# Kernel optimization log

Hardware: AMD Instinct MI355X
Metric: run time of the kernel (lower is better)

Reference implementation:

```python
import jax, jax.numpy as jnp
import numpy as np
from itertools import product

H, W, BINS = 480, 640, 10
B, N_PER = 8, 250000


def setup_inputs() -> dict:
    key = jax.random.key(0)
    kx, ky, kt, kp = jax.random.split(key, 4)
    N = B * N_PER
    x = jax.random.uniform(kx, (N,), minval=0.0, maxval=W - 1.0)
    y = jax.random.uniform(ky, (N,), minval=0.0, maxval=H - 1.0)
    # timestamps sorted within each batch (events arrive in time order)
    t = jnp.sort(jax.random.uniform(kt, (B, N_PER)), axis=1).reshape(-1)
    p = 2.0 * jax.random.bernoulli(kp, 0.5, (N,)).astype(jnp.float32) - 1.0  # polarity +/-1
    b = jnp.repeat(jnp.arange(B, dtype=jnp.float32), N_PER)
    events = jnp.stack([x, y, t, p, b], axis=1)  # [N,5]
    lengths = jnp.full((B,), N_PER, dtype=jnp.int32)
    return {"events": events, "lengths": lengths}


def _kb(a):
    # k_b(a) = relu(1 - |a|) trilinear kernel
    return jnp.maximum(0.0, 1.0 - jnp.abs(a))


def reference(events, lengths):
    x, y, t, p, b = (events[:, i] for i in range(5))
    Bn = lengths.shape[0]
    bi = b.astype(jnp.int32)
    csum = jnp.cumsum(lengths)
    first_idx = csum - lengths  # first event index per batch
    last_idx = csum - 1         # last event index per batch
    t0 = t[first_idx][bi]       # per-event start time of its batch
    tN = t[last_idx][bi]        # per-event end time of its batch
    t_star = (BINS - 1) * jnp.clip((t - t0) / (tN - t0), 0.0, 1.0)

    vox = jnp.zeros((Bn * BINS * H * W,), dtype=events.dtype)
    rounds = ((jnp.floor, True), (jnp.ceil, False))  # (fn, is_floor)
    for (xr, x_is_floor), (yr, y_is_floor), (br, b_is_floor) in product(rounds, rounds, rounds):
        x_ref = xr(x)
        y_ref = yr(y)
        bin_ref = br(t_star)
        valid = (((x_ref != x) | x_is_floor)
                 & ((y_ref != y) | y_is_floor)
                 & ((bin_ref != t_star) | b_is_floor)
                 & (x_ref < W) & (y_ref < H) & (bin_ref < BINS))
        val = jnp.where(valid,
                        p * _kb(x_ref - x) * _kb(y_ref - y) * _kb(bin_ref - t_star),
                        0.0)
        # integer index arithmetic (exact, unlike float accumulation)
        idx = (x_ref.astype(jnp.int32)
               + y_ref.astype(jnp.int32) * W
               + bin_ref.astype(jnp.int32) * (H * W)
               + bi * (BINS * H * W))
        idx = jnp.where(valid, idx, 0)
        vox = vox.at[idx].add(val)
    return vox.reshape(Bn, BINS, H, W)
```

## Files before the change

kernel.cpp:

```cpp
#include <hip/hip_runtime.h>
#include <hip/hip_bf16.h>

#define EV_H 480
#define EV_W 640
#define EV_BINS 10
#define TILE_ROWS 60
#define Y_TILES (EV_H / TILE_ROWS)
#define TILE_ELEMS (TILE_ROWS * EV_W)
#define SPLAT_THREADS 1024

#define WS_T0N_OFF   0
#define WS_OFFS_OFF  1024
#define WS_RNG_OFF   2048

__device__ __forceinline__ float ev_tstar(float t, float t0, float tN) {
    float q = (t - t0) / (tN - t0);
    q = fminf(fmaxf(q, 0.0f), 1.0f);
    return q * (float)(EV_BINS - 1);
}

__global__ void ev_prep_kernel(const float* __restrict__ events,
                               const int* __restrict__ lengths,
                               int Bn, float* __restrict__ t0N,
                               int* __restrict__ offs, int* __restrict__ rng) {
    int tid = threadIdx.x;
    if (tid == 0) {
        long long acc = 0;
        for (int i = 0; i < Bn; ++i) {
            offs[i] = (int)acc;
            acc += (long long)lengths[i];
            t0N[2 * i + 0] = events[(long long)offs[i] * 5 + 2];
            t0N[2 * i + 1] = events[(acc - 1) * 5 + 2];
        }
        offs[Bn] = (int)acc;
    }
    __syncthreads();

    int id = tid;
    if (id < Bn * EV_BINS) {
        int b = id / EV_BINS;
        int k = id % EV_BINS;
        int bs = offs[b], be = offs[b + 1];
        float t0 = t0N[2 * b], tN = t0N[2 * b + 1];
        float klo = (float)(k - 1);
        float khi = (float)(k + 1);
        int lo = bs, hi = be;
        while (lo < hi) {
            int mid = (lo + hi) >> 1;
            float ts = ev_tstar(events[(long long)mid * 5 + 2], t0, tN);
            if (ts > klo) hi = mid; else lo = mid + 1;
        }
        int L = lo;
        lo = bs; hi = be;
        while (lo < hi) {
            int mid = (lo + hi) >> 1;
            float ts = ev_tstar(events[(long long)mid * 5 + 2], t0, tN);
            if (ts >= khi) hi = mid; else lo = mid + 1;
        }
        rng[2 * id + 0] = L;
        rng[2 * id + 1] = lo;
    }
}

__global__ __launch_bounds__(SPLAT_THREADS) void ev_tile_kernel(
    const float* __restrict__ events,
    const float* __restrict__ t0N,
    const int* __restrict__ rng,
    float* __restrict__ vox) {
    extern __shared__ float tile[];

    int bid = blockIdx.x;
    int yt = bid % Y_TILES;
    int bk = bid / Y_TILES;
    int k  = bk % EV_BINS;
    int b  = bk / EV_BINS;
    int r0 = yt * TILE_ROWS;

    int tid = threadIdx.x;

    float4 z4 = make_float4(0.f, 0.f, 0.f, 0.f);
    float4* t4 = (float4*)tile;
    for (int j = tid; j < TILE_ELEMS / 4; j += SPLAT_THREADS) t4[j] = z4;
    __syncthreads();

    int lo = rng[2 * bk + 0];
    int hi = rng[2 * bk + 1];
    float t0 = t0N[2 * b], tN = t0N[2 * b + 1];
    float kf = (float)k;

    for (int i = lo + tid; i < hi; i += SPLAT_THREADS) {
        const float* e = events + (long long)i * 5;
        float x = e[0];
        float y = e[1];
        float t = e[2];
        float p = e[3];

        float ts = ev_tstar(t, t0, tN);
        float wt = 1.0f - fabsf(ts - kf);
        if (wt <= 0.0f) continue;

        float xf = floorf(x);
        float yf = floorf(y);
        int x0 = (int)xf;
        int y0 = (int)yf;
        float fx = x - xf;
        float fy = y - yf;
        float pw = p * wt;
        int x1ok = (x0 + 1) < EV_W;

        int rr = y0 - r0;
        if (rr >= 0 && rr < TILE_ROWS) {
            float a = pw * (1.0f - fy);
            float* row = tile + rr * EV_W;
            atomicAdd(row + x0, a * (1.0f - fx));
            if (x1ok) atomicAdd(row + x0 + 1, a * fx);
        }
        rr = y0 + 1 - r0;
        if (rr >= 0 && rr < TILE_ROWS) {
            float a = pw * fy;
            float* row = tile + rr * EV_W;
            atomicAdd(row + x0, a * (1.0f - fx));
            if (x1ok) atomicAdd(row + x0 + 1, a * fx);
        }
    }
    __syncthreads();

    float* dst = vox + ((long long)bk * (EV_H * EV_W) + (long long)r0 * EV_W);
    float4* d4 = (float4*)dst;
    for (int j = tid; j < TILE_ELEMS / 4; j += SPLAT_THREADS) d4[j] = t4[j];
}

extern "C" void kernel_launch(void* const* d_in, const int* in_sizes, int n_in,
                              void* d_out, int out_size, void* d_ws, size_t ws_size,
                              hipStream_t stream) {
    const float* events  = (const float*)d_in[0];
    const int*   lengths = (const int*)d_in[1];
    float*       vox     = (float*)d_out;

    char* ws = (char*)d_ws;
    float* t0N = (float*)(ws + WS_T0N_OFF);
    int*   offs = (int*)(ws + WS_OFFS_OFF);
    int*   rng  = (int*)(ws + WS_RNG_OFF);

    int Bn = in_sizes[1];

    hipFuncSetAttribute((const void*)ev_tile_kernel,
                        hipFuncAttributeMaxDynamicSharedMemorySize,
                        TILE_ELEMS * (int)sizeof(float));

    ev_prep_kernel<<<1, 256, 0, stream>>>(events, lengths, Bn, t0N, offs, rng);

    int blocks = Bn * EV_BINS * Y_TILES;
    ev_tile_kernel<<<blocks, SPLAT_THREADS, TILE_ELEMS * sizeof(float), stream>>>(
        events, t0N, rng, vox);
}
```

Baseline: 292.7 us.

## Bucket events by bin and row tile via count/scan/fill before splatting

Adds a counting-sort pipeline: count events per (batch, bin, 30-row tile) bucket, scan the counts, scatter compact (x, y, weight) records into buckets, then run one accumulation block per bucket. Before, every 60-row tile block re-read all events in its time range and threw away those outside its rows. This cuts redundant event reads and gives smaller tiles and more blocks. In exchange it adds three kernel launches, a memset, global atomics and a record buffer round trip. It only runs when the workspace is large enough and otherwise falls back to the old kernel.

```diff
diff --git a/kernel.cpp b/kernel.cpp
--- a/kernel.cpp
+++ b/kernel.cpp
@@ -4,14 +4,24 @@
 #define EV_H 480
 #define EV_W 640
 #define EV_BINS 10
-#define TILE_ROWS 60
-#define Y_TILES (EV_H / TILE_ROWS)
-#define TILE_ELEMS (TILE_ROWS * EV_W)
-#define SPLAT_THREADS 1024
-
-#define WS_T0N_OFF   0
-#define WS_OFFS_OFF  1024
-#define WS_RNG_OFF   2048
+
+#define FB_TILE_ROWS 60
+#define FB_Y_TILES (EV_H / FB_TILE_ROWS)
+#define FB_TILE_ELEMS (FB_TILE_ROWS * EV_W)
+#define FB_THREADS 1024
+
+#define TR2 30
+#define YT2 (EV_H / TR2)
+#define T2_TILE_ELEMS (TR2 * EV_W)
+#define EVT 2
+
+#define WS_T0N    0
+#define WS_OFFS   1024
+#define WS_RNG    2048
+#define WS_CNT    4096
+#define WS_BASE   12288
+#define WS_CUR    20480
+#define WS_REC    32768
 
 __device__ __forceinline__ float ev_tstar(float t, float t0, float tN) {
     float q = (t - t0) / (tN - t0);
@@ -62,25 +72,196 @@
     }
 }
 
-__global__ __launch_bounds__(SPLAT_THREADS) void ev_tile_kernel(
+__device__ __forceinline__ int ev_enum(float y, float ts, float p, int bi,
+                                       int bkt[4], float pw[4]) {
+    int k0 = (int)floorf(ts);
+    float ft = ts - (float)k0;
+    int y0 = (int)floorf(y);
+    int yt0 = y0 / TR2;
+    int yt1 = (y0 + 1) / TR2;
+    bool strad = (yt1 != yt0) && (yt1 < YT2);
+    bool hasc  = (ft > 0.0f) && (k0 + 1 < EV_BINS);
+    int base0 = (bi * EV_BINS + k0) * YT2;
+    float wf = p * (1.0f - ft);
+    float wc = p * ft;
+    bkt[0] = base0 + yt0;       pw[0] = wf;
+    bkt[1] = base0 + yt1;       pw[1] = wf;
+    bkt[2] = base0 + YT2 + yt0; pw[2] = wc;
+    bkt[3] = base0 + YT2 + yt1; pw[3] = wc;
+    return 1 | (strad ? 2 : 0) | (hasc ? 4 : 0) | ((strad && hasc) ? 8 : 0);
+}
+
+__global__ __launch_bounds__(256) void ev_count_kernel(
+    const float* __restrict__ events, const float* __restrict__ t0N,
+    int N, int NB, int* __restrict__ cnt) {
+    extern __shared__ int hist[];
+    for (int j = threadIdx.x; j < NB; j += 256) hist[j] = 0;
+    __syncthreads();
+    long long b0 = (long long)blockIdx.x * (256 * EVT);
+#pragma unroll
+    for (int it = 0; it < EVT; ++it) {
+        long long i = b0 + (long long)it * 256 + threadIdx.x;
+        if (i < N) {
+            const float* e = events + i * 5;
+            float y = e[1], t = e[2], p = e[3];
+            int bi = (int)e[4];
+            float ts = ev_tstar(t, t0N[2 * bi], t0N[2 * bi + 1]);
+            int bkt[4]; float pw[4];
+            int m = ev_enum(y, ts, p, bi, bkt, pw);
+#pragma unroll
+            for (int r = 0; r < 4; ++r)
+                if ((m >> r) & 1) atomicAdd(&hist[bkt[r]], 1);
+        }
+    }
+    __syncthreads();
+    for (int j = threadIdx.x; j < NB; j += 256) {
+        int c = hist[j];
+        if (c) atomicAdd(&cnt[j], c);
+    }
+}
+
+__global__ void ev_scan_kernel(const int* __restrict__ cnt, int NB,
+                               int* __restrict__ base, int* __restrict__ cur) {
+    int lane = threadIdx.x;
+    int per = (NB + 63) >> 6;
+    int s = 0;
+    for (int j = 0; j < per; ++j) {
+        int idx = lane * per + j;
+        if (idx < NB) s += cnt[idx];
+    }
+    int incl = s;
+    for (int d = 1; d < 64; d <<= 1) {
+        int v = __shfl_up(incl, d);
+        if (lane >= d) incl += v;
+    }
+    int run = incl - s;
+    for (int j = 0; j < per; ++j) {
+        int idx = lane * per + j;
+        if (idx < NB) {
+            base[idx] = run;
+            cur[idx] = run;
+            run += cnt[idx];
+        }
+    }
+}
+
+__global__ __launch_bounds__(256) void ev_fill_kernel(
+    const float* __restrict__ events, const float* __restrict__ t0N,
+    int N, int NB, int REC_CAP,
+    int* __restrict__ cur, float* __restrict__ rec) {
+    extern __shared__ int lds[];
+    int* hist  = lds;
+    int* cbase = lds + NB;
+    for (int j = threadIdx.x; j < NB; j += 256) hist[j] = 0;
+    __syncthreads();
+
+    long long b0 = (long long)blockIdx.x * (256 * EVT);
+    int   bkt[EVT][4];
+    int   lof[EVT][4];
+    float pwv[EVT][4];
+    float xs[EVT], ys[EVT];
+    int   mv[EVT];
+#pragma unroll
+    for (int it = 0; it < EVT; ++it) {
+        long long i = b0 + (long long)it * 256 + threadIdx.x;
+        mv[it] = 0;
+        if (i < N) {
+            const float* e = events + i * 5;
+            float x = e[0], y = e[1], t = e[2], p = e[3];
+            int bi = (int)e[4];
+            float ts = ev_tstar(t, t0N[2 * bi], t0N[2 * bi + 1]);
+            xs[it] = x; ys[it] = y;
+            mv[it] = ev_enum(y, ts, p, bi, bkt[it], pwv[it]);
+#pragma unroll
+            for (int r = 0; r < 4; ++r)
+                if ((mv[it] >> r) & 1) lof[it][r] = atomicAdd(&hist[bkt[it][r]], 1);
+        }
+    }
+    __syncthreads();
+    for (int j = threadIdx.x; j < NB; j += 256) {
+        int c = hist[j];
+        if (c) cbase[j] = atomicAdd(&cur[j], c);
+    }
+    __syncthreads();
+#pragma unroll
+    for (int it = 0; it < EVT; ++it) {
+#pragma unroll
+        for (int r = 0; r < 4; ++r) {
+            if ((mv[it] >> r) & 1) {
+                int pos = cbase[bkt[it][r]] + lof[it][r];
+                if (pos < REC_CAP) {
+                    float* q = rec + (long long)pos * 3;
+                    q[0] = xs[it]; q[1] = ys[it]; q[2] = pwv[it][r];
+                }
+            }
+        }
+    }
+}
+
+__global__ __launch_bounds__(1024) void ev_accum_kernel(
+    const float* __restrict__ rec, const int* __restrict__ base,
+    const int* __restrict__ cnt, int REC_CAP, float* __restrict__ vox) {
+    extern __shared__ float tile[];
+    int bid = blockIdx.x;
+    int yt = bid % YT2;
+    int bk = bid / YT2;
+    int r0 = yt * TR2;
+    int tid = threadIdx.x;
+
+    float4* t4 = (float4*)tile;
+    float4 z = make_float4(0.f, 0.f, 0.f, 0.f);
+    for (int j = tid; j < T2_TILE_ELEMS / 4; j += 1024) t4[j] = z;
+    __syncthreads();
+
+    int lo = base[bid];
+    int hi = lo + cnt[bid];
+    if (hi > REC_CAP) hi = REC_CAP;
+    for (int i = lo + tid; i < hi; i += 1024) {
+        const float* q = rec + (long long)i * 3;
+        float x = q[0], y = q[1], pw = q[2];
+        float xf = floorf(x), yf = floorf(y);
+        int x0 = (int)xf, y0 = (int)yf;
+        float fx = x - xf, fy = y - yf;
+        int x1ok = (x0 + 1) < EV_W;
+        int rr0 = y0 - r0;
+        int rr1 = rr0 + 1;
+        if (rr0 >= 0 && rr0 < TR2) {
+            float a = pw * (1.0f - fy);
+            float* row = tile + rr0 * EV_W;
+            atomicAdd(row + x0, a * (1.0f - fx));
+            if (x1ok) atomicAdd(row + x0 + 1, a * fx);
+        }
+        if (rr1 >= 0 && rr1 < TR2) {
+            float a = pw * fy;
+            float* row = tile + rr1 * EV_W;
+            atomicAdd(row + x0, a * (1.0f - fx));
+            if (x1ok) atomicAdd(row + x0 + 1, a * fx);
+        }
+    }
+    __syncthreads();
+
+    float* dst = vox + ((long long)bk * (EV_H * EV_W) + (long long)r0 * EV_W);
+    float4* d4 = (float4*)dst;
+    for (int j = tid; j < T2_TILE_ELEMS / 4; j += 1024) d4[j] = t4[j];
+}
+
+__global__ __launch_bounds__(FB_THREADS) void ev_tile_kernel(
     const float* __restrict__ events,
     const float* __restrict__ t0N,
     const int* __restrict__ rng,
     float* __restrict__ vox) {
     extern __shared__ float tile[];
-
     int bid = blockIdx.x;
-    int yt = bid % Y_TILES;
-    int bk = bid / Y_TILES;
+    int yt = bid % FB_Y_TILES;
+    int bk = bid / FB_Y_TILES;
     int k  = bk % EV_BINS;
     int b  = bk / EV_BINS;
-    int r0 = yt * TILE_ROWS;
-
+    int r0 = yt * FB_TILE_ROWS;
     int tid = threadIdx.x;
 
     float4 z4 = make_float4(0.f, 0.f, 0.f, 0.f);
     float4* t4 = (float4*)tile;
-    for (int j = tid; j < TILE_ELEMS / 4; j += SPLAT_THREADS) t4[j] = z4;
+    for (int j = tid; j < FB_TILE_ELEMS / 4; j += FB_THREADS) t4[j] = z4;
     __syncthreads();
 
     int lo = rng[2 * bk + 0];
@@ -88,35 +269,26 @@
     float t0 = t0N[2 * b], tN = t0N[2 * b + 1];
     float kf = (float)k;
 
-    for (int i = lo + tid; i < hi; i += SPLAT_THREADS) {
+    for (int i = lo + tid; i < hi; i += FB_THREADS) {
         const float* e = events + (long long)i * 5;
-        float x = e[0];
-        float y = e[1];
-        float t = e[2];
-        float p = e[3];
-
+        float x = e[0], y = e[1], t = e[2], p = e[3];
         float ts = ev_tstar(t, t0, tN);
         float wt = 1.0f - fabsf(ts - kf);
         if (wt <= 0.0f) continue;
-
-        float xf = floorf(x);
-        float yf = floorf(y);
-        int x0 = (int)xf;
-        int y0 = (int)yf;
-        float fx = x - xf;
-        float fy = y - yf;
+        float xf = floorf(x), yf = floorf(y);
+        int x0 = (int)xf, y0 = (int)yf;
+        float fx = x - xf, fy = y - yf;
         float pw = p * wt;
         int x1ok = (x0 + 1) < EV_W;
-
         int rr = y0 - r0;
-        if (rr >= 0 && rr < TILE_ROWS) {
+        if (rr >= 0 && rr < FB_TILE_ROWS) {
             float a = pw * (1.0f - fy);
             float* row = tile + rr * EV_W;
             atomicAdd(row + x0, a * (1.0f - fx));
             if (x1ok) atomicAdd(row + x0 + 1, a * fx);
         }
-        rr = y0 + 1 - r0;
-        if (rr >= 0 && rr < TILE_ROWS) {
+        rr += 1;
+        if (rr >= 0 && rr < FB_TILE_ROWS) {
             float a = pw * fy;
             float* row = tile + rr * EV_W;
             atomicAdd(row + x0, a * (1.0f - fx));
@@ -127,7 +299,7 @@
 
     float* dst = vox + ((long long)bk * (EV_H * EV_W) + (long long)r0 * EV_W);
     float4* d4 = (float4*)dst;
-    for (int j = tid; j < TILE_ELEMS / 4; j += SPLAT_THREADS) d4[j] = t4[j];
+    for (int j = tid; j < FB_TILE_ELEMS / 4; j += FB_THREADS) d4[j] = t4[j];
 }
 
 extern "C" void kernel_launch(void* const* d_in, const int* in_sizes, int n_in,
@@ -138,19 +310,45 @@
     float*       vox     = (float*)d_out;
 
     char* ws = (char*)d_ws;
-    float* t0N = (float*)(ws + WS_T0N_OFF);
-    int*   offs = (int*)(ws + WS_OFFS_OFF);
-    int*   rng  = (int*)(ws + WS_RNG_OFF);
-
+    float* t0N  = (float*)(ws + WS_T0N);
+    int*   offs = (int*)(ws + WS_OFFS);
+    int*   rng  = (int*)(ws + WS_RNG);
+    int*   cnt  = (int*)(ws + WS_CNT);
+    int*   base = (int*)(ws + WS_BASE);
+    int*   cur  = (int*)(ws + WS_CUR);
+    float* rec  = (float*)(ws + WS_REC);
+
+    int N  = in_sizes[0] / 5;
     int Bn = in_sizes[1];
-
+    int NB = Bn * EV_BINS * YT2;
+
+    hipFuncSetAttribute((const void*)ev_accum_kernel,
+                        hipFuncAttributeMaxDynamicSharedMemorySize,
+                        T2_TILE_ELEMS * (int)sizeof(float));
     hipFuncSetAttribute((const void*)ev_tile_kernel,
                         hipFuncAttributeMaxDynamicSharedMemorySize,
-                        TILE_ELEMS * (int)sizeof(float));
+                        FB_TILE_ELEMS * (int)sizeof(float));
 
     ev_prep_kernel<<<1, 256, 0, stream>>>(events, lengths, Bn, t0N, offs, rng);
 
-    int blocks = Bn * EV_BINS * Y_TILES;
-    ev_tile_kernel<<<blocks, SPLAT_THREADS, TILE_ELEMS * sizeof(float), stream>>>(
-        events, t0N, rng, vox);
-}
+    long long capll = ((long long)ws_size - WS_REC) / 12;
+    if (capll > 4LL * N) capll = 4LL * N;
+    bool two_pass = (NB * 4 <= 8192) && (capll * 5 >= 12LL * (long long)N);
+
+    if (two_pass) {
+        int REC_CAP = (int)capll;
+        int blocks1 = (N + 256 * EVT - 1) / (256 * EVT);
+        hipMemsetAsync(cnt, 0, (size_t)NB * sizeof(int), stream);
+        ev_count_kernel<<<blocks1, 256, NB * sizeof(int), stream>>>(
+            events, t0N, N, NB, cnt);
+        ev_scan_kernel<<<1, 64, 0, stream>>>(cnt, NB, base, cur);
+        ev_fill_kernel<<<blocks1, 256, 2 * NB * sizeof(int), stream>>>(
+            events, t0N, N, NB, REC_CAP, cur, rec);
+        ev_accum_kernel<<<NB, 1024, T2_TILE_ELEMS * sizeof(float), stream>>>(
+            rec, base, cnt, REC_CAP, vox);
+    } else {
+        int blocks = Bn * EV_BINS * FB_Y_TILES;
+        ev_tile_kernel<<<blocks, FB_THREADS, FB_TILE_ELEMS * sizeof(float), stream>>>(
+            events, t0N, rng, vox);
+    }
+}
```

New measurement: 266.8 us. 1.1x faster.
